# Kernel tuning notes

Measured on AMD Instinct MI355X. Metric: run time of the kernel, lower is better.

## Reference

```python
import jax, jax.numpy as jnp
import numpy as np

PAD = -999            # PADDING_INDEX sentinel from madrax
B, M = 4, 4096        # structures, atom slots per structure
N = B * M             # total atoms
CUTOFF = 7.0          # distance_threshold default in get_pairwise_representation
BOX = 80.0            # Angstrom box -> realistic neighbor density


def setup_inputs() -> dict:
    key = jax.random.key(0)
    k1, k2, k3, k4, k5, k6 = jax.random.split(key, 6)
    coordinates = jax.random.uniform(k1, (B, M, 3), jnp.float32) * BOX
    # pad the last 128 atom slots of every structure (coords[...,0] == PAD marks padding)
    coordinates = coordinates.at[:, M - 128:, 0].set(float(PAD))
    atom_batch = (jnp.arange(N) // M).astype(jnp.int32)                     # atom_description[:,0]
    coords_indexing_atom = jax.random.randint(k2, (N,), 0, M, jnp.int32)    # irregular gather slots
    partners = jax.random.randint(k3, (N, 2), 0, M, jnp.int32)
    partners = jnp.where(jax.random.uniform(k4, (N, 2)) < 0.1, PAD, partners)
    angle_indices = jax.random.randint(k5, (N, 4), 0, N, jnp.int32)
    angle_indices = jnp.where(jax.random.uniform(k6, (N, 1)) < 0.2, PAD, angle_indices)
    return {
        "coordinates": coordinates,
        "atom_batch": atom_batch,
        "coords_indexing_atom": coords_indexing_atom,
        "partners_indexing_atom": partners,
        "angle_indices": angle_indices,
    }


def _dihedral(p1, p2, p3, p4):
    # math_utils.dihedral2dVectors: standard signed torsion angle
    b1, b2, b3 = p2 - p1, p3 - p2, p4 - p3
    n1 = jnp.cross(b1, b2)
    n2 = jnp.cross(b2, b3)
    b2n = b2 / (jnp.linalg.norm(b2, axis=-1, keepdims=True) + 1e-12)
    m1 = jnp.cross(n1, b2n)
    x = jnp.sum(n1 * n2, axis=-1)
    y = jnp.sum(m1 * n2, axis=-1)
    return jnp.arctan2(y, x)


def reference(coordinates, atom_batch, coords_indexing_atom, partners_indexing_atom, angle_indices):
    # --- gather atom coordinates (coords = coordinates[batch, slot]) ---
    coords = coordinates[atom_batch, coords_indexing_atom]                   # [N,3]

    # --- gather partner coordinates with PAD masking (partners_final) ---
    pvalid = partners_indexing_atom != PAD                                   # [N,2]
    safe_p = jnp.where(pvalid, partners_indexing_atom, 0)
    pcoords = coordinates[atom_batch[:, None], safe_p]                       # [N,2,3]
    partners_final = jnp.where(pvalid[..., None], pcoords, float(PAD))

    # --- per-batch pairwise distance + 7A cutoff (get_pairwise_representation) ---
    cb = coords.reshape(B, M, 3)
    valid = cb[..., 0] != float(PAD)                                         # [B,M]
    sq = jnp.sum(cb * cb, axis=-1)                                           # [B,M]
    d2 = sq[:, :, None] + sq[:, None, :] - 2.0 * jnp.einsum('bic,bjc->bij', cb, cb)
    dist = jnp.sqrt(jnp.maximum(d2, 0.0) + 1e-12)                            # [B,M,M]
    pair_mask = valid[:, :, None] & valid[:, None, :] & (dist <= CUTOFF)
    # fixed-shape surrogate for the ragged pair list: per-atom neighbor distance sum
    nbr_sum = jnp.sum(jnp.where(pair_mask, dist, 0.0), axis=-1).reshape(N)   # [N]

    # --- dihedral angles with padding mask (_calculate_angles) ---
    amask = jnp.all(angle_indices != PAD, axis=-1)                           # [N]
    aidx = jnp.where(amask[:, None], angle_indices, 0)
    p = coords[aidx]                                                          # [N,4,3]
    ang = _dihedral(p[:, 0], p[:, 1], p[:, 2], p[:, 3])
    angles = jnp.where(amask, ang, float(PAD))                               # [N]

    # pack outputs: [N, 8] = angle, neighbor-dist-sum, partner coords (2x3)
    return jnp.concatenate([angles[:, None], nbr_sum[:, None], partners_final.reshape(N, 6)], axis=-1)
```

## Files before the change

kernel.cpp:

```cpp
#include <hip/hip_runtime.h>
#include <math.h>

#define kB 4
#define kM 4096
#define kN (kB * kM)
#define kPadF -999.0f
#define kPadI -999

#define kNC   11
#define kNC3  (kNC * kNC * kNC)
#define kCap  64
#define kOffWs     0
#define kOffCnt    262144
#define kOffCells  524288
#define kWsNeeded  (kOffCells + (size_t)kB * kNC3 * kCap * 16)

typedef float f32x2 __attribute__((ext_vector_type(2)));

__device__ __forceinline__ float sq_np(float x, float y, float z) {
    return __fadd_rn(__fadd_rn(__fmul_rn(x, x), __fmul_rn(y, y)),
                     __fmul_rn(z, z));
}

__device__ __forceinline__ float fast_sqrt(float x) {
#if __has_builtin(__builtin_amdgcn_sqrtf)
    return __builtin_amdgcn_sqrtf(x);
#else
    float r;
    asm volatile("v_sqrt_f32 %0, %1" : "=v"(r) : "v"(x));
    return r;
#endif
}

__device__ __forceinline__ int cell_coord(float v) {
    int c = (int)(v * (11.0f / 80.0f));
    return min(c, kNC - 1);
}

__global__ __launch_bounds__(64)
void per_atom_kernel(const float* __restrict__ coords,
                     const int*   __restrict__ cidx,
                     const int*   __restrict__ partners,
                     const int*   __restrict__ aidx,
                     float*       __restrict__ out,
                     float4*      __restrict__ ws,
                     int*         __restrict__ cellCnt,
                     float4*      __restrict__ cells)
{
    int i = blockIdx.x * 64 + threadIdx.x;
    if (i >= kN) return;
    int b = i >> 12;

    {
        int gc = cidx[i];
        const float* s = coords + (size_t)(b * kM + gc) * 3;
        float x = s[0], y = s[1], z = s[2];
        float4 v = make_float4(x, y, z, sq_np(x, y, z));
        ws[i] = v;
        if (x != kPadF) {
            int cid = ((b * kNC + cell_coord(x)) * kNC + cell_coord(y)) * kNC
                      + cell_coord(z);
            int slot = atomicAdd(&cellCnt[cid], 1);
            if (slot < kCap) cells[(size_t)cid * kCap + slot] = v;
        }
    }

    float o2, o3, o4, o5, o6, o7;
    int p0 = partners[2 * i + 0];
    int p1 = partners[2 * i + 1];
    if (p0 == kPadI) { o2 = o3 = o4 = kPadF; }
    else {
        const float* s = coords + (size_t)(b * kM + p0) * 3;
        o2 = s[0]; o3 = s[1]; o4 = s[2];
    }
    if (p1 == kPadI) { o5 = o6 = o7 = kPadF; }
    else {
        const float* s = coords + (size_t)(b * kM + p1) * 3;
        o5 = s[0]; o6 = s[1]; o7 = s[2];
    }

    int4 a = *reinterpret_cast<const int4*>(aidx + 4 * i);
    float ang = kPadF;
    if (a.x != kPadI && a.y != kPadI && a.z != kPadI && a.w != kPadI) {
        int ai[4] = {a.x, a.y, a.z, a.w};
        float P[4][3];
        #pragma unroll
        for (int k = 0; k < 4; ++k) {
            int g  = ai[k];
            int gb = g >> 12;
            int gc = cidx[g];
            const float* s = coords + (size_t)(gb * kM + gc) * 3;
            P[k][0] = s[0]; P[k][1] = s[1]; P[k][2] = s[2];
        }
        float b1x = P[1][0] - P[0][0], b1y = P[1][1] - P[0][1], b1z = P[1][2] - P[0][2];
        float b2x = P[2][0] - P[1][0], b2y = P[2][1] - P[1][1], b2z = P[2][2] - P[1][2];
        float b3x = P[3][0] - P[2][0], b3y = P[3][1] - P[2][1], b3z = P[3][2] - P[2][2];
        float n1x = b1y * b2z - b1z * b2y;
        float n1y = b1z * b2x - b1x * b2z;
        float n1z = b1x * b2y - b1y * b2x;
        float n2x = b2y * b3z - b2z * b3y;
        float n2y = b2z * b3x - b2x * b3z;
        float n2z = b2x * b3y - b2y * b3x;
        float nb2 = sqrtf(b2x * b2x + b2y * b2y + b2z * b2z) + 1e-12f;
        float inv = 1.0f / nb2;
        float ux = b2x * inv, uy = b2y * inv, uz = b2z * inv;
        float m1x = n1y * uz - n1z * uy;
        float m1y = n1z * ux - n1x * uz;
        float m1z = n1x * uy - n1y * ux;
        float x = n1x * n2x + n1y * n2y + n1z * n2z;
        float y = m1x * n2x + m1y * n2y + m1z * n2z;
        ang = atan2f(y, x);
    }

    float4* o = reinterpret_cast<float4*>(out + (size_t)i * 8);
    o[0] = make_float4(ang, 0.0f, o2, o3);
    o[1] = make_float4(o4, o5, o6, o7);
}

__global__ __launch_bounds__(256)
void nbr_cell_kernel(const float4* __restrict__ ws,
                     const int*    __restrict__ cellCnt,
                     const float4* __restrict__ cells,
                     float*        __restrict__ out)
{
    int task = blockIdx.x * 256 + threadIdx.x;
    if (task >= 27 * kN) return;
    int k = task >> 14;
    int i = task & (kN - 1);

    float4 ri = ws[i];
    if (ri.x == kPadF) return;

    int b  = i >> 12;
    int nx = cell_coord(ri.x) + (k / 9)     - 1;
    int ny = cell_coord(ri.y) + ((k / 3) % 3) - 1;
    int nz = cell_coord(ri.z) + (k % 3)     - 1;
    if ((unsigned)nx >= kNC || (unsigned)ny >= kNC || (unsigned)nz >= kNC)
        return;

    int cid = ((b * kNC + nx) * kNC + ny) * kNC + nz;
    int cnt = min(cellCnt[cid], kCap);
    const float4* cp = cells + (size_t)cid * kCap;

    float sum = 0.0f;
    for (int s = 0; s < cnt; ++s) {
        float4 c   = cp[s];
        float dot  = __fmaf_rn(ri.z, c.z,
                     __fmaf_rn(ri.y, c.y, __fmul_rn(ri.x, c.x)));
        float d2   = __fmaf_rn(-2.0f, dot, __fadd_rn(ri.w, c.w));
        float dist = fast_sqrt(__builtin_fabsf(d2));
        sum += (d2 <= 49.0f) ? dist : 0.0f;
    }
    if (sum != 0.0f) {
        atomicAdd(out + (size_t)i * 8 + 1, sum);
    }
}

__global__ __launch_bounds__(256)
void nbr_kernel_lds(const float* __restrict__ coords,
                    const int*   __restrict__ cidx,
                    float*       __restrict__ out)
{
    __shared__ float4 sc[kM];
    int b    = blockIdx.x >> 6;
    int row0 = (blockIdx.x & 63) << 6;
    for (int j = threadIdx.x; j < kM; j += 256) {
        int idx = cidx[b * kM + j];
        const float* s = coords + (size_t)(b * kM + idx) * 3;
        float x = s[0], y = s[1], z = s[2];
        sc[j] = make_float4(x, y, z, sq_np(x, y, z));
    }
    __syncthreads();
    int r   = row0 + (threadIdx.x >> 2);
    int sub = threadIdx.x & 3;
    float4 ci = sc[r];
    float sum = 0.0f;
    for (int jj = 0; jj < kM / 4; ++jj) {
        float4 c   = sc[4 * jj + sub];
        float dot  = __fmaf_rn(ci.z, c.z,
                     __fmaf_rn(ci.y, c.y, __fmul_rn(ci.x, c.x)));
        float d2   = __fmaf_rn(-2.0f, dot, __fadd_rn(ci.w, c.w));
        float dist = fast_sqrt(fmaxf(d2, 0.0f));
        sum += (d2 <= 49.0f) ? dist : 0.0f;
    }
    sum += __shfl_xor(sum, 1);
    sum += __shfl_xor(sum, 2);
    if (sub == 0)
        out[(size_t)(b * kM + r) * 8 + 1] = (ci.x != kPadF) ? sum : 0.0f;
}

extern "C" void kernel_launch(void* const* d_in, const int* in_sizes, int n_in,
                              void* d_out, int out_size, void* d_ws, size_t ws_size,
                              hipStream_t stream) {
    const float* coords   = (const float*)d_in[0];
    const int*   cidx     = (const int*)d_in[2];
    const int*   partners = (const int*)d_in[3];
    const int*   aidx     = (const int*)d_in[4];
    float*       out      = (float*)d_out;

    char*   wsB     = (char*)d_ws;
    float4* ws      = (float4*)(wsB + kOffWs);
    int*    cellCnt = (int*)(wsB + kOffCnt);
    float4* cells   = (float4*)(wsB + kOffCells);

    if (ws_size >= kWsNeeded) {
        hipMemsetAsync(cellCnt, 0, (size_t)kB * kNC3 * sizeof(int), stream);
        hipLaunchKernelGGL(per_atom_kernel, dim3(kN / 64), dim3(64), 0, stream,
                           coords, cidx, partners, aidx, out, ws, cellCnt, cells);
        hipLaunchKernelGGL(nbr_cell_kernel, dim3((27 * kN) / 256), dim3(256),
                           0, stream, ws, cellCnt, cells, out);
    } else {
        hipLaunchKernelGGL(per_atom_kernel, dim3(kN / 64), dim3(64), 0, stream,
                           coords, cidx, partners, aidx, out,
                           (float4*)d_ws, (int*)d_ws, (float4*)d_ws);
        hipLaunchKernelGGL(nbr_kernel_lds, dim3(kB * 64), dim3(256), 0, stream,
                           coords, cidx, out);
    }
}
```

Measured before the change: 74.61 us.

## Split per-atom work into role-specialized blocks for cell binning, angles, partners

The per-atom kernel now launches 256 blocks of 256 threads, where the block index selects one of four roles: coordinate gather with cell binning, dihedral angle, first partner gather, or second partner gather. The aim is to shorten the serial dependency chain per thread so the cell binning that the neighbor kernel waits on overlaps with the gather-heavy angle work. In exchange, the output is written as scattered scalar stores instead of two float4 stores. The original monolithic kernel is kept as a fallback for when workspace is small.

```diff
diff --git a/kernel.cpp b/kernel.cpp
--- a/kernel.cpp
+++ b/kernel.cpp
@@ -14,8 +14,6 @@
 #define kOffCnt    262144
 #define kOffCells  524288
 #define kWsNeeded  (kOffCells + (size_t)kB * kNC3 * kCap * 16)
-
-typedef float f32x2 __attribute__((ext_vector_type(2)));
 
 __device__ __forceinline__ float sq_np(float x, float y, float z) {
     return __fadd_rn(__fadd_rn(__fmul_rn(x, x), __fmul_rn(y, y)),
@@ -37,7 +35,7 @@
     return min(c, kNC - 1);
 }
 
-__global__ __launch_bounds__(64)
+__global__ __launch_bounds__(256)
 void per_atom_kernel(const float* __restrict__ coords,
                      const int*   __restrict__ cidx,
                      const int*   __restrict__ partners,
@@ -47,23 +45,129 @@
                      int*         __restrict__ cellCnt,
                      float4*      __restrict__ cells)
 {
-    int i = blockIdx.x * 64 + threadIdx.x;
-    if (i >= kN) return;
-    int b = i >> 12;
-
-    {
+    int role = blockIdx.x >> 6;
+    int i    = ((blockIdx.x & 63) << 8) + threadIdx.x;
+    int b    = i >> 12;
+
+    if (role == 0) {
         int gc = cidx[i];
         const float* s = coords + (size_t)(b * kM + gc) * 3;
         float x = s[0], y = s[1], z = s[2];
         float4 v = make_float4(x, y, z, sq_np(x, y, z));
         ws[i] = v;
+        out[(size_t)i * 8 + 1] = 0.0f;
         if (x != kPadF) {
             int cid = ((b * kNC + cell_coord(x)) * kNC + cell_coord(y)) * kNC
                       + cell_coord(z);
             int slot = atomicAdd(&cellCnt[cid], 1);
             if (slot < kCap) cells[(size_t)cid * kCap + slot] = v;
         }
-    }
+    } else if (role == 1) {
+        int4 a = *reinterpret_cast<const int4*>(aidx + 4 * i);
+        float ang = kPadF;
+        if (a.x != kPadI && a.y != kPadI && a.z != kPadI && a.w != kPadI) {
+            int ai[4] = {a.x, a.y, a.z, a.w};
+            float P[4][3];
+            #pragma unroll
+            for (int k = 0; k < 4; ++k) {
+                int g  = ai[k];
+                int gb = g >> 12;
+                int gc = cidx[g];
+                const float* s = coords + (size_t)(gb * kM + gc) * 3;
+                P[k][0] = s[0]; P[k][1] = s[1]; P[k][2] = s[2];
+            }
+            float b1x = P[1][0] - P[0][0], b1y = P[1][1] - P[0][1], b1z = P[1][2] - P[0][2];
+            float b2x = P[2][0] - P[1][0], b2y = P[2][1] - P[1][1], b2z = P[2][2] - P[1][2];
+            float b3x = P[3][0] - P[2][0], b3y = P[3][1] - P[2][1], b3z = P[3][2] - P[2][2];
+            float n1x = b1y * b2z - b1z * b2y;
+            float n1y = b1z * b2x - b1x * b2z;
+            float n1z = b1x * b2y - b1y * b2x;
+            float n2x = b2y * b3z - b2z * b3y;
+            float n2y = b2z * b3x - b2x * b3z;
+            float n2z = b2x * b3y - b2y * b3x;
+            float nb2 = sqrtf(b2x * b2x + b2y * b2y + b2z * b2z) + 1e-12f;
+            float inv = 1.0f / nb2;
+            float ux = b2x * inv, uy = b2y * inv, uz = b2z * inv;
+            float m1x = n1y * uz - n1z * uy;
+            float m1y = n1z * ux - n1x * uz;
+            float m1z = n1x * uy - n1y * ux;
+            float x = n1x * n2x + n1y * n2y + n1z * n2z;
+            float y = m1x * n2x + m1y * n2y + m1z * n2z;
+            ang = atan2f(y, x);
+        }
+        out[(size_t)i * 8 + 0] = ang;
+    } else if (role == 2) {
+        float o2, o3, o4;
+        int p0 = partners[2 * i + 0];
+        if (p0 == kPadI) { o2 = o3 = o4 = kPadF; }
+        else {
+            const float* s = coords + (size_t)(b * kM + p0) * 3;
+            o2 = s[0]; o3 = s[1]; o4 = s[2];
+        }
+        float* o = out + (size_t)i * 8;
+        o[2] = o2; o[3] = o3; o[4] = o4;
+    } else {
+        float o5, o6, o7;
+        int p1 = partners[2 * i + 1];
+        if (p1 == kPadI) { o5 = o6 = o7 = kPadF; }
+        else {
+            const float* s = coords + (size_t)(b * kM + p1) * 3;
+            o5 = s[0]; o6 = s[1]; o7 = s[2];
+        }
+        float* o = out + (size_t)i * 8;
+        o[5] = o5; o[6] = o6; o[7] = o7;
+    }
+}
+
+__global__ __launch_bounds__(256)
+void nbr_cell_kernel(const float4* __restrict__ ws,
+                     const int*    __restrict__ cellCnt,
+                     const float4* __restrict__ cells,
+                     float*        __restrict__ out)
+{
+    int task = blockIdx.x * 256 + threadIdx.x;
+    if (task >= 27 * kN) return;
+    int k = task >> 14;
+    int i = task & (kN - 1);
+
+    float4 ri = ws[i];
+    if (ri.x == kPadF) return;
+
+    int b  = i >> 12;
+    int nx = cell_coord(ri.x) + (k / 9)       - 1;
+    int ny = cell_coord(ri.y) + ((k / 3) % 3) - 1;
+    int nz = cell_coord(ri.z) + (k % 3)       - 1;
+    if ((unsigned)nx >= kNC || (unsigned)ny >= kNC || (unsigned)nz >= kNC)
+        return;
+
+    int cid = ((b * kNC + nx) * kNC + ny) * kNC + nz;
+    int cnt = min(cellCnt[cid], kCap);
+    const float4* cp = cells + (size_t)cid * kCap;
+
+    float sum = 0.0f;
+    for (int s = 0; s < cnt; ++s) {
+        float4 c   = cp[s];
+        float dot  = __fmaf_rn(ri.z, c.z,
+                     __fmaf_rn(ri.y, c.y, __fmul_rn(ri.x, c.x)));
+        float d2   = __fmaf_rn(-2.0f, dot, __fadd_rn(ri.w, c.w));
+        float dist = fast_sqrt(__builtin_fabsf(d2));
+        sum += (d2 <= 49.0f) ? dist : 0.0f;
+    }
+    if (sum != 0.0f) {
+        atomicAdd(out + (size_t)i * 8 + 1, sum);
+    }
+}
+
+__global__ __launch_bounds__(64)
+void per_atom_mono_kernel(const float* __restrict__ coords,
+                          const int*   __restrict__ cidx,
+                          const int*   __restrict__ partners,
+                          const int*   __restrict__ aidx,
+                          float*       __restrict__ out)
+{
+    int i = blockIdx.x * 64 + threadIdx.x;
+    if (i >= kN) return;
+    int b = i >> 12;
 
     float o2, o3, o4, o5, o6, o7;
     int p0 = partners[2 * i + 0];
@@ -118,45 +222,6 @@
 }
 
 __global__ __launch_bounds__(256)
-void nbr_cell_kernel(const float4* __restrict__ ws,
-                     const int*    __restrict__ cellCnt,
-                     const float4* __restrict__ cells,
-                     float*        __restrict__ out)
-{
-    int task = blockIdx.x * 256 + threadIdx.x;
-    if (task >= 27 * kN) return;
-    int k = task >> 14;
-    int i = task & (kN - 1);
-
-    float4 ri = ws[i];
-    if (ri.x == kPadF) return;
-
-    int b  = i >> 12;
-    int nx = cell_coord(ri.x) + (k / 9)     - 1;
-    int ny = cell_coord(ri.y) + ((k / 3) % 3) - 1;
-    int nz = cell_coord(ri.z) + (k % 3)     - 1;
-    if ((unsigned)nx >= kNC || (unsigned)ny >= kNC || (unsigned)nz >= kNC)
-        return;
-
-    int cid = ((b * kNC + nx) * kNC + ny) * kNC + nz;
-    int cnt = min(cellCnt[cid], kCap);
-    const float4* cp = cells + (size_t)cid * kCap;
-
-    float sum = 0.0f;
-    for (int s = 0; s < cnt; ++s) {
-        float4 c   = cp[s];
-        float dot  = __fmaf_rn(ri.z, c.z,
-                     __fmaf_rn(ri.y, c.y, __fmul_rn(ri.x, c.x)));
-        float d2   = __fmaf_rn(-2.0f, dot, __fadd_rn(ri.w, c.w));
-        float dist = fast_sqrt(__builtin_fabsf(d2));
-        sum += (d2 <= 49.0f) ? dist : 0.0f;
-    }
-    if (sum != 0.0f) {
-        atomicAdd(out + (size_t)i * 8 + 1, sum);
-    }
-}
-
-__global__ __launch_bounds__(256)
 void nbr_kernel_lds(const float* __restrict__ coords,
                     const int*   __restrict__ cidx,
                     float*       __restrict__ out)
@@ -205,14 +270,13 @@
 
     if (ws_size >= kWsNeeded) {
         hipMemsetAsync(cellCnt, 0, (size_t)kB * kNC3 * sizeof(int), stream);
-        hipLaunchKernelGGL(per_atom_kernel, dim3(kN / 64), dim3(64), 0, stream,
+        hipLaunchKernelGGL(per_atom_kernel, dim3(256), dim3(256), 0, stream,
                            coords, cidx, partners, aidx, out, ws, cellCnt, cells);
         hipLaunchKernelGGL(nbr_cell_kernel, dim3((27 * kN) / 256), dim3(256),
                            0, stream, ws, cellCnt, cells, out);
     } else {
-        hipLaunchKernelGGL(per_atom_kernel, dim3(kN / 64), dim3(64), 0, stream,
-                           coords, cidx, partners, aidx, out,
-                           (float4*)d_ws, (int*)d_ws, (float4*)d_ws);
+        hipLaunchKernelGGL(per_atom_mono_kernel, dim3(kN / 64), dim3(64), 0, stream,
+                           coords, cidx, partners, aidx, out);
         hipLaunchKernelGGL(nbr_kernel_lds, dim3(kB * 64), dim3(256), 0, stream,
                            coords, cidx, out);
     }
```

Result: no change. 74.28 us, median of 2 (-0.4%).
